# Kernel tuning notes

Hardware: AMD Instinct MI355X
Metric: run time of the kernel (lower is better)

Reference implementation:

```python
import jax, jax.numpy as jnp
import numpy as np

B = 262144      # batch of states (PPO rollout)
J = 16          # num_pools -> state_dim=32, action_dim=256
M = 12          # num_epochs_per_day (experts)
H = 34          # hidden_dim (fixed in source)
A = J * J


def setup_inputs() -> dict:
    key = jax.random.key(0)
    ks = jax.random.split(key, 6)
    states = jax.random.normal(ks[0], (B, 2 * J), dtype=jnp.float32)
    epoch_idx = jax.random.randint(ks[1], (B,), 0, M, dtype=jnp.int32)
    # fc1: kaiming normal (relu), zero bias
    W1 = jax.random.normal(ks[2], (H, 2 * J), dtype=jnp.float32) * np.sqrt(2.0 / (2 * J))
    b1 = jnp.zeros((H,), dtype=jnp.float32)
    # m expert output layers [M, A, H]
    Wout = jax.random.normal(ks[3], (M, A, H), dtype=jnp.float32) * np.sqrt(1.0 / H)
    bout = jax.random.normal(ks[4], (M, A), dtype=jnp.float32) * np.sqrt(1.0 / H)
    mask = jax.random.randint(ks[5], (J, J), 0, 2, dtype=jnp.int32)
    return {"states": states, "epoch_idx": epoch_idx, "W1": W1, "b1": b1,
            "Wout": Wout, "bout": bout, "mask": mask}


def reference(states, epoch_idx, W1, b1, Wout, bout, mask):
    # shared trunk: [B, H]
    x = jax.nn.relu(jnp.einsum('bs,hs->bh', states, W1) + b1)
    # grouped expert GEMM via one-hot routing (equivalent to output_layers[epoch_idx])
    onehot = jax.nn.one_hot(epoch_idx, M, dtype=x.dtype)           # [B, M]
    xe = x[:, None, :] * onehot[:, :, None]                        # [B, M, H]
    logits = jnp.einsum('bmh,mah->ba', xe, Wout) + bout[epoch_idx]  # [B, A]
    logits = logits.reshape(-1, J, J)
    NEG = jnp.float32(-1e9)
    return jnp.where(mask == 0, NEG, logits)
```

## Files before the change

kernel.cpp:

```cpp
#include <hip/hip_runtime.h>

typedef __attribute__((ext_vector_type(8))) short short8;
typedef __attribute__((ext_vector_type(4))) float f32x4;
typedef __attribute__((ext_vector_type(4))) int   i32x4;

#define SDIM 32
#define HDIM 34
#define NEXP 12
#define ACOL 256
#define SPB  256
#define MAXROWS 432
#undef  MAXROWS
#define MAXROWS 448

__device__ __forceinline__ unsigned int bpack(float lo, float hi) {
    unsigned int a = __builtin_bit_cast(unsigned int, lo);
    unsigned int b = __builtin_bit_cast(unsigned int, hi);
    return ((a + 0x8000u) >> 16) | ((b + 0x8000u) & 0xffff0000u);
}

__global__ __launch_bounds__(256, 4) void actor_kernel(
    const float* __restrict__ states,
    const int*   __restrict__ epoch_idx,
    const float* __restrict__ W1,
    const float* __restrict__ b1,
    const float* __restrict__ Wout,
    const float* __restrict__ bout,
    const int*   __restrict__ mask,
    float*       __restrict__ out,
    int nB)
{
    __shared__ __align__(16) unsigned int xs[MAXROWS * 16];
    __shared__ unsigned int   xt[MAXROWS];
    __shared__ unsigned short rowid[MAXROWS];
    __shared__ float w1s[HDIM * SDIM];
    __shared__ float b1s[HDIM];
    __shared__ int   cnt[NEXP], goff[NEXP], ntl[NEXP];

    const int t  = threadIdx.x;
    const int s0 = blockIdx.x * SPB;

    for (int i = t; i < HDIM * SDIM; i += 256) w1s[i] = W1[i];
    if (t < HDIM) b1s[t] = b1[t];
    if (t < NEXP) cnt[t] = 0;
    for (int i = t; i < MAXROWS; i += 256) rowid[i] = 0xFFFFu;

    const int  sidx  = s0 + t;
    const bool valid = (sidx < nB);
    float sr[SDIM];
    int e = 0;
    if (valid) {
        const f32x4* sp = (const f32x4*)(states + (size_t)sidx * SDIM);
        #pragma unroll
        for (int q = 0; q < SDIM / 4; ++q) {
            f32x4 v = sp[q];
            sr[4*q+0] = v[0]; sr[4*q+1] = v[1]; sr[4*q+2] = v[2]; sr[4*q+3] = v[3];
        }
        e = epoch_idx[sidx];
    }
    __syncthreads();

    int rank = 0;
    if (valid) rank = atomicAdd(&cnt[e], 1);
    __syncthreads();

    if (t == 0) {
        int base = 0;
        #pragma unroll
        for (int i = 0; i < NEXP; ++i) {
            goff[i] = base;
            int nt = (cnt[i] + 15) >> 4;
            ntl[i] = nt;
            base += nt << 4;
        }
    }
    float x[HDIM];
    if (valid) {
        #pragma unroll 2
        for (int h = 0; h < HDIM; ++h) {
            float acc = b1s[h];
            const float4* wr = (const float4*)(w1s + h * SDIM);
            #pragma unroll
            for (int q = 0; q < SDIM / 4; ++q) {
                float4 wv = wr[q];
                acc = fmaf(sr[4*q+0], wv.x, acc);
                acc = fmaf(sr[4*q+1], wv.y, acc);
                acc = fmaf(sr[4*q+2], wv.z, acc);
                acc = fmaf(sr[4*q+3], wv.w, acc);
            }
            x[h] = fmaxf(acc, 0.0f);
        }
    }
    __syncthreads();

    if (valid) {
        const int slot = goff[e] + rank;
        const unsigned swz = (unsigned)(slot & 3) << 4;
        char* rbase = (char*)xs + slot * 64;
        unsigned d[16];
        #pragma unroll
        for (int k = 0; k < 16; ++k) d[k] = bpack(x[2*k], x[2*k+1]);
        #pragma unroll
        for (int c = 0; c < 4; ++c) {
            f32x4 q;
            q[0] = __builtin_bit_cast(float, d[4*c+0]);
            q[1] = __builtin_bit_cast(float, d[4*c+1]);
            q[2] = __builtin_bit_cast(float, d[4*c+2]);
            q[3] = __builtin_bit_cast(float, d[4*c+3]);
            *(f32x4*)(rbase + (((unsigned)(c * 16)) ^ swz)) = q;
        }
        xt[slot]    = bpack(x[32], x[33]);
        rowid[slot] = (unsigned short)t;
    }
    __syncthreads();

    const int wv   = t >> 6;
    const int lane = t & 63;
    const int r    = lane & 15;
    const int g    = lane >> 4;
    const int cb0  = wv * 64 + 4 * g;
    const float NEG = -1e9f;
    const float INF = __builtin_bit_cast(float, 0x7f800000u);

    f32x4 mf[4];
    #pragma unroll
    for (int j = 0; j < 4; ++j) {
        i32x4 mq = *(const i32x4*)(mask + cb0 + 16 * j);
        mf[j][0] = mq[0] ? INF : NEG;
        mf[j][1] = mq[1] ? INF : NEG;
        mf[j][2] = mq[2] ? INF : NEG;
        mf[j][3] = mq[3] ? INF : NEG;
    }

    float* outb = out + (size_t)s0 * ACOL;

    for (int e2 = 0; e2 < NEXP; ++e2) {
        const int ntiles = ntl[e2];
        if (ntiles == 0) continue;

        short8   bf1[4];
        unsigned w2[4];
        f32x4    bv[4];
        #pragma unroll
        for (int j = 0; j < 4; ++j) {
            const int col = wv * 64 + j * 16 + r;
            const float* wr = Wout + ((size_t)e2 * ACOL + col) * HDIM;
            const float2* wp = (const float2*)(wr + g * 8);
            float2 p0 = wp[0], p1 = wp[1], p2 = wp[2], p3 = wp[3];
            uint4 q1 = make_uint4(bpack(p0.x, p0.y), bpack(p1.x, p1.y),
                                  bpack(p2.x, p2.y), bpack(p3.x, p3.y));
            bf1[j] = __builtin_bit_cast(short8, q1);
            w2[j]  = (g == 0) ? bpack(wr[32], wr[33]) : 0u;
            bv[j]  = *(const f32x4*)(bout + e2 * ACOL + cb0 + 16 * j);
        }

        const int tb = goff[e2];
        for (int st = 0; st < ntiles; ++st) {
            const int row = tb + (st << 4) + r;
            const char* rp = (const char*)xs + row * 64;
            short8 a1 = *(const short8*)(rp + (((unsigned)(g * 16)) ^ ((unsigned)(row & 3) << 4)));
            const unsigned xtv = xt[row];
            const unsigned rid = rowid[row];
            short8 a2 = __builtin_bit_cast(short8,
                          make_uint4(g == 0 ? xtv : 0u, 0u, 0u, 0u));

            f32x4 acc[4];
            #pragma unroll
            for (int j = 0; j < 4; ++j) {
                f32x4 a = bv[j];
                a = __builtin_amdgcn_mfma_f32_16x16x32_bf16(bf1[j], a1, a, 0, 0, 0);
                short8 b2 = __builtin_bit_cast(short8,
                              make_uint4(w2[j], 0u, 0u, 0u));
                a = __builtin_amdgcn_mfma_f32_16x16x32_bf16(b2, a2, a, 0, 0, 0);
                acc[j] = a;
            }

            if (rid != 0xFFFFu) {
                float* ob = outb + (size_t)rid * ACOL + cb0;
                #pragma unroll
                for (int j = 0; j < 4; ++j) {
                    f32x4 v = acc[j];
                    v[0] = fminf(v[0], mf[j][0]);
                    v[1] = fminf(v[1], mf[j][1]);
                    v[2] = fminf(v[2], mf[j][2]);
                    v[3] = fminf(v[3], mf[j][3]);
                    *(f32x4*)(ob + 16 * j) = v;
                }
            }
        }
    }
}

extern "C" void kernel_launch(void* const* d_in, const int* in_sizes, int n_in,
                              void* d_out, int out_size, void* d_ws, size_t ws_size,
                              hipStream_t stream) {
    const float* states    = (const float*)d_in[0];
    const int*   epoch_idx = (const int*)  d_in[1];
    const float* W1        = (const float*)d_in[2];
    const float* b1        = (const float*)d_in[3];
    const float* Wout      = (const float*)d_in[4];
    const float* bout      = (const float*)d_in[5];
    const int*   mask      = (const int*)  d_in[6];
    float*       out       = (float*)d_out;

    const int nB   = in_sizes[0] / SDIM;
    const int grid = (nB + SPB - 1) / SPB;
    actor_kernel<<<grid, 256, 0, stream>>>(states, epoch_idx, W1, b1,
                                           Wout, bout, mask, out, nB);
}
```

Baseline: 103.6 us.

## Stage MFMA outputs through LDS for full-row coalesced nontemporal stores

```diff
diff --git a/kernel.cpp b/kernel.cpp
--- a/kernel.cpp
+++ b/kernel.cpp
@@ -9,9 +9,11 @@
 #define NEXP 12
 #define ACOL 256
 #define SPB  256
-#define MAXROWS 432
-#undef  MAXROWS
 #define MAXROWS 448
+#define STG_STRIDE 260
+
+#define BAR_RAW()  asm volatile("s_barrier" ::: "memory")
+#define BAR_LGKM() asm volatile("s_waitcnt lgkmcnt(0)\n\ts_barrier" ::: "memory")
 
 __device__ __forceinline__ unsigned int bpack(float lo, float hi) {
     unsigned int a = __builtin_bit_cast(unsigned int, lo);
@@ -19,7 +21,7 @@
     return ((a + 0x8000u) >> 16) | ((b + 0x8000u) & 0xffff0000u);
 }
 
-__global__ __launch_bounds__(256, 4) void actor_kernel(
+__global__ __launch_bounds__(256, 3) void actor_kernel(
     const float* __restrict__ states,
     const int*   __restrict__ epoch_idx,
     const float* __restrict__ W1,
@@ -33,9 +35,11 @@
     __shared__ __align__(16) unsigned int xs[MAXROWS * 16];
     __shared__ unsigned int   xt[MAXROWS];
     __shared__ unsigned short rowid[MAXROWS];
-    __shared__ float w1s[HDIM * SDIM];
-    __shared__ float b1s[HDIM];
-    __shared__ int   cnt[NEXP], goff[NEXP], ntl[NEXP];
+    __shared__ __align__(16) float stg[16 * STG_STRIDE];
+    __shared__ int cnt[NEXP], goff[NEXP], ntl[NEXP];
+
+    float* w1s = stg;
+    float* b1s = stg + HDIM * SDIM;
 
     const int t  = threadIdx.x;
     const int s0 = blockIdx.x * SPB;
@@ -95,7 +99,7 @@
 
     if (valid) {
         const int slot = goff[e] + rank;
-        const unsigned swz = (unsigned)(slot & 3) << 4;
+        const unsigned sw = (((unsigned)slot >> 2) & 3u) << 4;
         char* rbase = (char*)xs + slot * 64;
         unsigned d[16];
         #pragma unroll
@@ -107,7 +111,7 @@
             q[1] = __builtin_bit_cast(float, d[4*c+1]);
             q[2] = __builtin_bit_cast(float, d[4*c+2]);
             q[3] = __builtin_bit_cast(float, d[4*c+3]);
-            *(f32x4*)(rbase + (((unsigned)(c * 16)) ^ swz)) = q;
+            *(f32x4*)(rbase + (((unsigned)(c * 16)) ^ sw)) = q;
         }
         xt[slot]    = bpack(x[32], x[33]);
         rowid[slot] = (unsigned short)t;
@@ -118,19 +122,9 @@
     const int lane = t & 63;
     const int r    = lane & 15;
     const int g    = lane >> 4;
-    const int cb0  = wv * 64 + 4 * g;
+    const int colbase = wv * 64 + r;
     const float NEG = -1e9f;
-    const float INF = __builtin_bit_cast(float, 0x7f800000u);
-
-    f32x4 mf[4];
-    #pragma unroll
-    for (int j = 0; j < 4; ++j) {
-        i32x4 mq = *(const i32x4*)(mask + cb0 + 16 * j);
-        mf[j][0] = mq[0] ? INF : NEG;
-        mf[j][1] = mq[1] ? INF : NEG;
-        mf[j][2] = mq[2] ? INF : NEG;
-        mf[j][3] = mq[3] ? INF : NEG;
-    }
+    const i32x4 mq = *(const i32x4*)(mask + 4 * lane);
 
     float* outb = out + (size_t)s0 * ACOL;
 
@@ -140,10 +134,10 @@
 
         short8   bf1[4];
         unsigned w2[4];
-        f32x4    bv[4];
+        float    bias[4];
         #pragma unroll
         for (int j = 0; j < 4; ++j) {
-            const int col = wv * 64 + j * 16 + r;
+            const int col = colbase + j * 16;
             const float* wr = Wout + ((size_t)e2 * ACOL + col) * HDIM;
             const float2* wp = (const float2*)(wr + g * 8);
             float2 p0 = wp[0], p1 = wp[1], p2 = wp[2], p3 = wp[3];
@@ -151,41 +145,52 @@
                                   bpack(p2.x, p2.y), bpack(p3.x, p3.y));
             bf1[j] = __builtin_bit_cast(short8, q1);
             w2[j]  = (g == 0) ? bpack(wr[32], wr[33]) : 0u;
-            bv[j]  = *(const f32x4*)(bout + e2 * ACOL + cb0 + 16 * j);
+            bias[j] = bout[e2 * ACOL + col];
         }
 
         const int tb = goff[e2];
         for (int st = 0; st < ntiles; ++st) {
-            const int row = tb + (st << 4) + r;
+            const int rb  = tb + (st << 4);
+            const int row = rb + r;
+            const unsigned sw = (((unsigned)row >> 2) & 3u) << 4;
             const char* rp = (const char*)xs + row * 64;
-            short8 a1 = *(const short8*)(rp + (((unsigned)(g * 16)) ^ ((unsigned)(row & 3) << 4)));
-            const unsigned xtv = xt[row];
-            const unsigned rid = rowid[row];
+            short8 a1 = *(const short8*)(rp + (((unsigned)(g * 16)) ^ sw));
             short8 a2 = __builtin_bit_cast(short8,
-                          make_uint4(g == 0 ? xtv : 0u, 0u, 0u, 0u));
+                          make_uint4(g == 0 ? xt[row] : 0u, 0u, 0u, 0u));
 
             f32x4 acc[4];
             #pragma unroll
             for (int j = 0; j < 4; ++j) {
-                f32x4 a = bv[j];
-                a = __builtin_amdgcn_mfma_f32_16x16x32_bf16(bf1[j], a1, a, 0, 0, 0);
+                f32x4 a = {bias[j], bias[j], bias[j], bias[j]};
+                a = __builtin_amdgcn_mfma_f32_16x16x32_bf16(a1, bf1[j], a, 0, 0, 0);
                 short8 b2 = __builtin_bit_cast(short8,
                               make_uint4(w2[j], 0u, 0u, 0u));
-                a = __builtin_amdgcn_mfma_f32_16x16x32_bf16(b2, a2, a, 0, 0, 0);
+                a = __builtin_amdgcn_mfma_f32_16x16x32_bf16(a2, b2, a, 0, 0, 0);
                 acc[j] = a;
             }
 
-            if (rid != 0xFFFFu) {
-                float* ob = outb + (size_t)rid * ACOL + cb0;
+            BAR_RAW();
+            #pragma unroll
+            for (int j = 0; j < 4; ++j) {
+                const int c = colbase + 16 * j;
                 #pragma unroll
-                for (int j = 0; j < 4; ++j) {
-                    f32x4 v = acc[j];
-                    v[0] = fminf(v[0], mf[j][0]);
-                    v[1] = fminf(v[1], mf[j][1]);
-                    v[2] = fminf(v[2], mf[j][2]);
-                    v[3] = fminf(v[3], mf[j][3]);
-                    *(f32x4*)(ob + 16 * j) = v;
-                }
+                for (int i = 0; i < 4; ++i)
+                    stg[(g * 4 + i) * STG_STRIDE + c] = acc[j][i];
+            }
+            BAR_LGKM();
+
+            #pragma unroll
+            for (int q = 0; q < 4; ++q) {
+                const int lrow = wv * 4 + q;
+                const unsigned rid = rowid[rb + lrow];
+                f32x4 v = *(const f32x4*)&stg[lrow * STG_STRIDE + 4 * lane];
+                v[0] = mq[0] ? v[0] : NEG;
+                v[1] = mq[1] ? v[1] : NEG;
+                v[2] = mq[2] ? v[2] : NEG;
+                v[3] = mq[3] ? v[3] : NEG;
+                if (rid != 0xFFFFu)
+                    __builtin_nontemporal_store(v,
+                        (f32x4*)(outb + (size_t)rid * ACOL + 4 * lane));
             }
         }
     }
```

After: 101.1 us. 2.4% less time.

## Split into global expert-sort pipeline: count, scan, trunk-scatter, grouped GEMM

Applied to the files above, without the earlier changes.

```diff
diff --git a/kernel.cpp b/kernel.cpp
--- a/kernel.cpp
+++ b/kernel.cpp
@@ -2,16 +2,11 @@
 
 typedef __attribute__((ext_vector_type(8))) short short8;
 typedef __attribute__((ext_vector_type(4))) float f32x4;
-typedef __attribute__((ext_vector_type(4))) int   i32x4;
 
 #define SDIM 32
 #define HDIM 34
 #define NEXP 12
 #define ACOL 256
-#define SPB  256
-#define MAXROWS 432
-#undef  MAXROWS
-#define MAXROWS 448
 
 __device__ __forceinline__ unsigned int bpack(float lo, float hi) {
     unsigned int a = __builtin_bit_cast(unsigned int, lo);
@@ -19,33 +14,66 @@
     return ((a + 0x8000u) >> 16) | ((b + 0x8000u) & 0xffff0000u);
 }
 
-__global__ __launch_bounds__(256, 4) void actor_kernel(
-    const float* __restrict__ states,
-    const int*   __restrict__ epoch_idx,
-    const float* __restrict__ W1,
-    const float* __restrict__ b1,
-    const float* __restrict__ Wout,
-    const float* __restrict__ bout,
-    const int*   __restrict__ mask,
-    float*       __restrict__ out,
-    int nB)
-{
-    __shared__ __align__(16) unsigned int xs[MAXROWS * 16];
-    __shared__ unsigned int   xt[MAXROWS];
-    __shared__ unsigned short rowid[MAXROWS];
+__global__ __launch_bounds__(256) void k1_count(
+    const int* __restrict__ epoch_idx, int* __restrict__ cnts, int nB)
+{
+    __shared__ int lc[NEXP];
+    const int t = threadIdx.x;
+    if (t < NEXP) lc[t] = 0;
+    __syncthreads();
+    const int sidx = blockIdx.x * 256 + t;
+    if (sidx < nB) atomicAdd(&lc[epoch_idx[sidx]], 1);
+    __syncthreads();
+    if (t < NEXP) cnts[blockIdx.x * NEXP + t] = lc[t];
+}
+
+__global__ __launch_bounds__(256) void k2_scan(
+    const int* __restrict__ cnts, int* __restrict__ hist,
+    int* __restrict__ cb, int* __restrict__ cur, int nblk)
+{
+    __shared__ int part[NEXP][17];
+    const int t = threadIdx.x;
+    const int e = t >> 4, p = t & 15;
+    if (e < NEXP) {
+        int s = 0;
+        #pragma unroll 4
+        for (int b = p; b < nblk; b += 16) s += cnts[b * NEXP + e];
+        part[e][p] = s;
+    }
+    __syncthreads();
+    if (t < NEXP) {
+        int h = 0;
+        #pragma unroll
+        for (int q = 0; q < 16; ++q) h += part[t][q];
+        hist[t] = h;
+        cur[t]  = 0;
+    }
+    __syncthreads();
+    if (t == 0) {
+        int c = 0;
+        #pragma unroll
+        for (int i = 0; i < NEXP; ++i) { cb[i] = c; c += (hist[i] + 255) >> 8; }
+        cb[NEXP] = c;
+    }
+}
+
+__global__ __launch_bounds__(256) void k3_trunk(
+    const float* __restrict__ states, const int* __restrict__ epoch_idx,
+    const float* __restrict__ W1, const float* __restrict__ b1,
+    const int* __restrict__ cb, int* __restrict__ cur,
+    uint4* __restrict__ xg, unsigned int* __restrict__ xtg,
+    int* __restrict__ idxg, int nB)
+{
     __shared__ float w1s[HDIM * SDIM];
     __shared__ float b1s[HDIM];
-    __shared__ int   cnt[NEXP], goff[NEXP], ntl[NEXP];
-
-    const int t  = threadIdx.x;
-    const int s0 = blockIdx.x * SPB;
-
+    __shared__ int lc[NEXP], lbase[NEXP], lcb[NEXP];
+
+    const int t = threadIdx.x;
     for (int i = t; i < HDIM * SDIM; i += 256) w1s[i] = W1[i];
     if (t < HDIM) b1s[t] = b1[t];
-    if (t < NEXP) cnt[t] = 0;
-    for (int i = t; i < MAXROWS; i += 256) rowid[i] = 0xFFFFu;
-
-    const int  sidx  = s0 + t;
+    if (t < NEXP) lc[t] = 0;
+
+    const int  sidx  = blockIdx.x * 256 + t;
     const bool valid = (sidx < nB);
     float sr[SDIM];
     int e = 0;
@@ -61,18 +89,12 @@
     __syncthreads();
 
     int rank = 0;
-    if (valid) rank = atomicAdd(&cnt[e], 1);
-    __syncthreads();
-
-    if (t == 0) {
-        int base = 0;
-        #pragma unroll
-        for (int i = 0; i < NEXP; ++i) {
-            goff[i] = base;
-            int nt = (cnt[i] + 15) >> 4;
-            ntl[i] = nt;
-            base += nt << 4;
-        }
+    if (valid) rank = atomicAdd(&lc[e], 1);
+    __syncthreads();
+
+    if (t < NEXP) {
+        lbase[t] = atomicAdd(&cur[t], lc[t]);
+        lcb[t]   = cb[t];
     }
     float x[HDIM];
     if (valid) {
@@ -94,98 +116,97 @@
     __syncthreads();
 
     if (valid) {
-        const int slot = goff[e] + rank;
-        const unsigned swz = (unsigned)(slot & 3) << 4;
-        char* rbase = (char*)xs + slot * 64;
-        unsigned d[16];
-        #pragma unroll
-        for (int k = 0; k < 16; ++k) d[k] = bpack(x[2*k], x[2*k+1]);
-        #pragma unroll
-        for (int c = 0; c < 4; ++c) {
-            f32x4 q;
-            q[0] = __builtin_bit_cast(float, d[4*c+0]);
-            q[1] = __builtin_bit_cast(float, d[4*c+1]);
-            q[2] = __builtin_bit_cast(float, d[4*c+2]);
-            q[3] = __builtin_bit_cast(float, d[4*c+3]);
-            *(f32x4*)(rbase + (((unsigned)(c * 16)) ^ swz)) = q;
-        }
-        xt[slot]    = bpack(x[32], x[33]);
-        rowid[slot] = (unsigned short)t;
-    }
-    __syncthreads();
-
-    const int wv   = t >> 6;
-    const int lane = t & 63;
-    const int r    = lane & 15;
-    const int g    = lane >> 4;
-    const int cb0  = wv * 64 + 4 * g;
+        const int slot = (lcb[e] << 8) + lbase[e] + rank;
+        unsigned d[17];
+        #pragma unroll
+        for (int k = 0; k < 17; ++k) d[k] = bpack(x[2*k], x[2*k+1]);
+        uint4* xr = xg + (size_t)slot * 4;
+        xr[0] = make_uint4(d[0],  d[1],  d[2],  d[3]);
+        xr[1] = make_uint4(d[4],  d[5],  d[6],  d[7]);
+        xr[2] = make_uint4(d[8],  d[9],  d[10], d[11]);
+        xr[3] = make_uint4(d[12], d[13], d[14], d[15]);
+        xtg[slot]  = d[16];
+        idxg[slot] = sidx;
+    }
+}
+
+__global__ __launch_bounds__(256, 4) void k4_gemm(
+    const float* __restrict__ Wout, const float* __restrict__ bout,
+    const int* __restrict__ mask,
+    const uint4* __restrict__ xg, const unsigned int* __restrict__ xtg,
+    const int* __restrict__ idxg,
+    const int* __restrict__ cb, const int* __restrict__ hist,
+    float* __restrict__ out)
+{
+    __shared__ float stg[4][16 * 68];
+
+    const int bh   = blockIdx.x;
+    const int b    = bh >> 1;
+    const int half = bh & 1;
+    if (b >= cb[NEXP]) return;
+
+    int e = 0;
+    while (e < NEXP - 1 && b >= cb[e + 1]) ++e;
+    int nvalid = hist[e] - ((b - cb[e]) << 8);
+    if (nvalid > 256) nvalid = 256;
+    const int ntt = (nvalid + 15) >> 4;
+    const int st0 = half * 8;
+    const int st1 = (st0 + 8 < ntt) ? st0 + 8 : ntt;
+    if (st0 >= st1) return;
+
+    const int t = threadIdx.x;
+    const int wv = t >> 6, lane = t & 63;
+    const int r = lane & 15, g = lane >> 4;
+    const int m = mask[wv * 64 + lane];
     const float NEG = -1e9f;
-    const float INF = __builtin_bit_cast(float, 0x7f800000u);
-
-    f32x4 mf[4];
+
+    short8   bf[4];
+    unsigned w2[4];
+    float    bias[4];
     #pragma unroll
     for (int j = 0; j < 4; ++j) {
-        i32x4 mq = *(const i32x4*)(mask + cb0 + 16 * j);
-        mf[j][0] = mq[0] ? INF : NEG;
-        mf[j][1] = mq[1] ? INF : NEG;
-        mf[j][2] = mq[2] ? INF : NEG;
-        mf[j][3] = mq[3] ? INF : NEG;
-    }
-
-    float* outb = out + (size_t)s0 * ACOL;
-
-    for (int e2 = 0; e2 < NEXP; ++e2) {
-        const int ntiles = ntl[e2];
-        if (ntiles == 0) continue;
-
-        short8   bf1[4];
-        unsigned w2[4];
-        f32x4    bv[4];
+        const int col = wv * 64 + j * 16 + r;
+        const float* wr = Wout + ((size_t)e * ACOL + col) * HDIM;
+        const float2* wp = (const float2*)(wr + g * 8);
+        float2 p0 = wp[0], p1 = wp[1], p2 = wp[2], p3 = wp[3];
+        uint4 q1 = make_uint4(bpack(p0.x, p0.y), bpack(p1.x, p1.y),
+                              bpack(p2.x, p2.y), bpack(p3.x, p3.y));
+        bf[j]  = __builtin_bit_cast(short8, q1);
+        w2[j]  = (g == 0) ? bpack(wr[32], wr[33]) : 0u;
+        bias[j] = bout[e * ACOL + col];
+    }
+
+    const uint4*        xb   = xg   + ((size_t)b << 10);
+    const unsigned int* xtb  = xtg  + (b << 8);
+    const int*          idxb = idxg + (b << 8);
+    float* mystg = stg[wv];
+
+    for (int st = st0; st < st1; ++st) {
+        const int rb  = st << 4;
+        const int row = rb + r;
+        short8 a1 = __builtin_bit_cast(short8, xb[row * 4 + g]);
+        const unsigned xtv = (g == 0) ? xtb[row] : 0u;
+        short8 a2 = __builtin_bit_cast(short8, make_uint4(xtv, 0u, 0u, 0u));
+
         #pragma unroll
         for (int j = 0; j < 4; ++j) {
-            const int col = wv * 64 + j * 16 + r;
-            const float* wr = Wout + ((size_t)e2 * ACOL + col) * HDIM;
-            const float2* wp = (const float2*)(wr + g * 8);
-            float2 p0 = wp[0], p1 = wp[1], p2 = wp[2], p3 = wp[3];
-            uint4 q1 = make_uint4(bpack(p0.x, p0.y), bpack(p1.x, p1.y),
-                                  bpack(p2.x, p2.y), bpack(p3.x, p3.y));
-            bf1[j] = __builtin_bit_cast(short8, q1);
-            w2[j]  = (g == 0) ? bpack(wr[32], wr[33]) : 0u;
-            bv[j]  = *(const f32x4*)(bout + e2 * ACOL + cb0 + 16 * j);
-        }
-
-        const int tb = goff[e2];
-        for (int st = 0; st < ntiles; ++st) {
-            const int row = tb + (st << 4) + r;
-            const char* rp = (const char*)xs + row * 64;
-            short8 a1 = *(const short8*)(rp + (((unsigned)(g * 16)) ^ ((unsigned)(row & 3) << 4)));
-            const unsigned xtv = xt[row];
-            const unsigned rid = rowid[row];
-            short8 a2 = __builtin_bit_cast(short8,
-                          make_uint4(g == 0 ? xtv : 0u, 0u, 0u, 0u));
-
-            f32x4 acc[4];
+            f32x4 a = {bias[j], bias[j], bias[j], bias[j]};
+            a = __builtin_amdgcn_mfma_f32_16x16x32_bf16(a1, bf[j], a, 0, 0, 0);
+            short8 b2 = __builtin_bit_cast(short8, make_uint4(w2[j], 0u, 0u, 0u));
+            a = __builtin_amdgcn_mfma_f32_16x16x32_bf16(a2, b2, a, 0, 0, 0);
             #pragma unroll
-            for (int j = 0; j < 4; ++j) {
-                f32x4 a = bv[j];
-                a = __builtin_amdgcn_mfma_f32_16x16x32_bf16(bf1[j], a1, a, 0, 0, 0);
-                short8 b2 = __builtin_bit_cast(short8,
-                              make_uint4(w2[j], 0u, 0u, 0u));
-                a = __builtin_amdgcn_mfma_f32_16x16x32_bf16(b2, a2, a, 0, 0, 0);
-                acc[j] = a;
-            }
-
-            if (rid != 0xFFFFu) {
-                float* ob = outb + (size_t)rid * ACOL + cb0;
-                #pragma unroll
-                for (int j = 0; j < 4; ++j) {
-                    f32x4 v = acc[j];
-                    v[0] = fminf(v[0], mf[j][0]);
-                    v[1] = fminf(v[1], mf[j][1]);
-                    v[2] = fminf(v[2], mf[j][2]);
-                    v[3] = fminf(v[3], mf[j][3]);
-                    *(f32x4*)(ob + 16 * j) = v;
-                }
+            for (int i = 0; i < 4; ++i)
+                mystg[(4 * g + i) * 68 + 16 * j + r] = a[i];
+        }
+
+        const int nrow = nvalid - rb;
+        #pragma unroll
+        for (int lrow = 0; lrow < 16; ++lrow) {
+            if (lrow < nrow) {
+                const int rid = idxb[rb + lrow];
+                float v = mystg[lrow * 68 + lane];
+                v = m ? v : NEG;
+                out[(size_t)rid * ACOL + wv * 64 + lane] = v;
             }
         }
     }
@@ -203,8 +224,26 @@
     const int*   mask      = (const int*)  d_in[6];
     float*       out       = (float*)d_out;
 
-    const int nB   = in_sizes[0] / SDIM;
-    const int grid = (nB + SPB - 1) / SPB;
-    actor_kernel<<<grid, 256, 0, stream>>>(states, epoch_idx, W1, b1,
-                                           Wout, bout, mask, out, nB);
-}
+    const int nB       = in_sizes[0] / SDIM;
+    const int nblk     = (nB + 255) / 256;
+    const int nchk_max = nblk + NEXP;
+
+    char* ws = (char*)d_ws;
+    int* hist = (int*)(ws + 0);
+    int* cb   = (int*)(ws + 64);
+    int* cur  = (int*)(ws + 128);
+    int* cnts = (int*)(ws + 256);
+    size_t o_idx = 256 + (((size_t)nblk * NEXP * 4 + 255) & ~(size_t)255);
+    size_t o_xt  = o_idx + (((size_t)nchk_max * 1024 + 255) & ~(size_t)255);
+    size_t o_x   = o_xt  + (((size_t)nchk_max * 1024 + 255) & ~(size_t)255);
+    int*          idxg = (int*)(ws + o_idx);
+    unsigned int* xtg  = (unsigned int*)(ws + o_xt);
+    uint4*        xg   = (uint4*)(ws + o_x);
+
+    k1_count<<<nblk, 256, 0, stream>>>(epoch_idx, cnts, nB);
+    k2_scan<<<1, 256, 0, stream>>>(cnts, hist, cb, cur, nblk);
+    k3_trunk<<<nblk, 256, 0, stream>>>(states, epoch_idx, W1, b1,
+                                       cb, cur, xg, xtg, idxg, nB);
+    k4_gemm<<<nchk_max * 2, 256, 0, stream>>>(Wout, bout, mask,
+                                              xg, xtg, idxg, cb, hist, out);
+}
```

After: 116.7 us. 1.13x slower.
